# Kernel tuning notes

Hardware: AMD Instinct MI355X
Metric: run time of the kernel (lower is better)

The kernel has to match this reference:

```python
import jax, jax.numpy as jnp
import numpy as np

IN_CH, HID = 602, 256
N0, N1, N2 = 256000, 10240, 1024
E1, E2 = 256000, 10240


def setup_inputs() -> dict:
    key = jax.random.key(0)
    ks = jax.random.split(key, 12)
    x = jax.random.normal(ks[0], (N0, IN_CH), dtype=jnp.float32)
    src1 = jax.random.randint(ks[1], (E1,), 0, N0)
    dst1 = jax.random.randint(ks[2], (E1,), 0, N1)
    src2 = jax.random.randint(ks[3], (E2,), 0, N1)
    dst2 = jax.random.randint(ks[4], (E2,), 0, N2)
    s1 = 1.0 / np.sqrt(IN_CH)
    s2 = 1.0 / np.sqrt(HID)
    W1l = jax.random.normal(ks[5], (IN_CH, HID), dtype=jnp.float32) * s1
    W1r = jax.random.normal(ks[6], (IN_CH, HID), dtype=jnp.float32) * s1
    b1 = jax.random.normal(ks[7], (HID,), dtype=jnp.float32) * s1
    W2l = jax.random.normal(ks[8], (HID, HID), dtype=jnp.float32) * s2
    W2r = jax.random.normal(ks[9], (HID, HID), dtype=jnp.float32) * s2
    b2 = jax.random.normal(ks[10], (HID,), dtype=jnp.float32) * s2
    return {"x": x, "src1": src1, "dst1": dst1, "src2": src2, "dst2": dst2,
            "W1l": W1l, "b1": b1, "W1r": W1r, "W2l": W2l, "b2": b2, "W2r": W2r,
            "n1": N1, "n2": N2}


def _sage_mean(x_src, x_tgt, src, dst, Wl, bl, Wr, n_tgt):
    # gather neighbor (source) features, mean-aggregate to targets
    msg = x_src[src]  # [E, C]
    ssum = jax.ops.segment_sum(msg, dst, num_segments=n_tgt)
    cnt = jax.ops.segment_sum(jnp.ones((src.shape[0], 1), x_src.dtype), dst,
                              num_segments=n_tgt)
    agg = ssum / jnp.maximum(cnt, 1.0)  # isolated targets get 0 (PyG scatter-mean)
    # SAGEConv: lin_l(agg) (with bias) + lin_r(x_root) (no bias)
    return agg @ Wl + bl + x_tgt @ Wr


def reference(x, src1, dst1, src2, dst2, W1l, b1, W1r, W2l, b2, W2r, n1, n2):
    h = _sage_mean(x, x[:n1], src1, dst1, W1l, b1, W1r, n1)
    h = jax.nn.relu(h)  # dropout p=0.5 is identity in eval mode
    out = _sage_mean(h, h[:n2], src2, dst2, W2l, b2, W2r, n2)
    return out
```

## Files before the change

kernel.cpp:

```cpp
#include <hip/hip_runtime.h>
#include <hip/hip_bf16.h>

#define IN_CH 602
#define HID 256
#define N0C 256000
#define N1C 10240
#define N2C 1024
#define E1C 256000
#define E2C 10240
#define K1 1216
#define K2 512

typedef __bf16 bf16x8 __attribute__((ext_vector_type(8)));
typedef float f32x4 __attribute__((ext_vector_type(4)));
typedef unsigned short u16;


__global__ void hist_kernel(const int* __restrict__ dst, int* __restrict__ cnt, int E) {
    int i = blockIdx.x * blockDim.x + threadIdx.x;
    if (i < E) atomicAdd(&cnt[dst[i]], 1);
}

__global__ void scan_kernel(const int* __restrict__ cnt, int* __restrict__ offs,
                            int* __restrict__ cursor, int n) {
    __shared__ int part[256];
    int tid = threadIdx.x;
    int chunk = n >> 8;
    int lo = tid * chunk;
    int s = 0;
    for (int i = 0; i < chunk; i++) s += cnt[lo + i];
    part[tid] = s;
    __syncthreads();
    for (int d = 1; d < 256; d <<= 1) {
        int v = (tid >= d) ? part[tid - d] : 0;
        __syncthreads();
        part[tid] += v;
        __syncthreads();
    }
    int run = part[tid] - s;
    for (int i = 0; i < chunk; i++) {
        offs[lo + i] = run;
        cursor[lo + i] = run;
        run += cnt[lo + i];
    }
}

__global__ void fill_kernel(const int* __restrict__ src, const int* __restrict__ dst,
                            int* __restrict__ cursor, int* __restrict__ eidx, int E) {
    int i = blockIdx.x * blockDim.x + threadIdx.x;
    if (i < E) {
        int p = atomicAdd(&cursor[dst[i]], 1);
        eidx[p] = src[i];
    }
}


__global__ void build_bt_kernel(const float* __restrict__ Wl, const float* __restrict__ Wr,
                                __hip_bfloat16* __restrict__ Bt, int Kin, int Kpad) {
    int idx = blockIdx.x * blockDim.x + threadIdx.x;
    int total = HID * Kpad;
    if (idx >= total) return;
    int n = idx / Kpad, k = idx - n * Kpad;
    float v = 0.f;
    if (k < Kin)            v = Wl[k * HID + n];
    else if (k < 2 * Kin)   v = Wr[(k - Kin) * HID + n];
    Bt[(size_t)n * Kpad + k] = __float2bfloat16(v);
}


__global__ void agg1_kernel(const float* __restrict__ x, const int* __restrict__ cnt,
                            const int* __restrict__ offs, const int* __restrict__ eidx,
                            __hip_bfloat16* __restrict__ A1) {
    int t = blockIdx.x;
    int tid = threadIdx.x;
    int deg = cnt[t];
    int base = offs[t];
    float a0 = 0.f, a1 = 0.f, a2 = 0.f;
    for (int i = 0; i < deg; i++) {
        const float* row = x + (size_t)eidx[base + i] * IN_CH;
        a0 += row[tid];
        if (tid < IN_CH - 256) a1 += row[tid + 256];
        if (tid < IN_CH - 512) a2 += row[tid + 512];
    }
    float inv = 1.0f / (float)(deg > 0 ? deg : 1);
    __hip_bfloat16* d = A1 + (size_t)t * K1;
    d[tid] = __float2bfloat16(a0 * inv);
    if (tid < IN_CH - 256) d[tid + 256] = __float2bfloat16(a1 * inv);
    if (tid < IN_CH - 512) d[tid + 512] = __float2bfloat16(a2 * inv);
    const float* xr = x + (size_t)t * IN_CH;
    d[IN_CH + tid] = __float2bfloat16(xr[tid]);
    if (tid < IN_CH - 256) d[IN_CH + tid + 256] = __float2bfloat16(xr[tid + 256]);
    if (tid < IN_CH - 512) d[IN_CH + tid + 512] = __float2bfloat16(xr[tid + 512]);
    if (tid < K1 - 2 * IN_CH) d[2 * IN_CH + tid] = __float2bfloat16(0.f);
}


__global__ void agg2_kernel(const __hip_bfloat16* __restrict__ h, const int* __restrict__ cnt,
                            const int* __restrict__ offs, const int* __restrict__ eidx,
                            __hip_bfloat16* __restrict__ A2) {
    int t = blockIdx.x, tid = threadIdx.x;
    int deg = cnt[t], base = offs[t];
    float acc = 0.f;
    for (int i = 0; i < deg; i++)
        acc += __bfloat162float(h[(size_t)eidx[base + i] * HID + tid]);
    float inv = 1.0f / (float)(deg > 0 ? deg : 1);
    A2[(size_t)t * K2 + tid] = __float2bfloat16(acc * inv);
    A2[(size_t)t * K2 + HID + tid] = h[(size_t)t * HID + tid];
}


template <int K, bool RELU, bool OUT_BF16>
__global__ __launch_bounds__(256) void gemm_kernel(const __hip_bfloat16* __restrict__ A,
                                                   const __hip_bfloat16* __restrict__ Bt,
                                                   const float* __restrict__ bias,
                                                   void* __restrict__ Cout) {
    __shared__ __align__(16) u16 As[128 * 40];
    __shared__ __align__(16) u16 Bs[128 * 40];
    int tid = threadIdx.x;
    int m0 = blockIdx.x * 128;
    int n0 = blockIdx.y * 128;
    int wave = tid >> 6, lane = tid & 63;
    int wm = (wave & 1) * 64, wn = (wave >> 1) * 64;
    int lm = lane & 15, quad = lane >> 4;
    int k8 = quad * 8;
    int sr = tid >> 2;
    int sc = (tid & 3) * 8;
    const u16* Au = (const u16*)A;
    const u16* Bu = (const u16*)Bt;

    f32x4 acc[4][4];
#pragma unroll
    for (int i = 0; i < 4; i++)
#pragma unroll
        for (int j = 0; j < 4; j++) acc[i][j] = (f32x4){0.f, 0.f, 0.f, 0.f};

    for (int kt = 0; kt < K; kt += 32) {
#pragma unroll
        for (int hh = 0; hh < 2; hh++) {
            int r = sr + 64 * hh;
            *(uint4*)&As[r * 40 + sc] = *(const uint4*)&Au[(size_t)(m0 + r) * K + kt + sc];
            *(uint4*)&Bs[r * 40 + sc] = *(const uint4*)&Bu[(size_t)(n0 + r) * K + kt + sc];
        }
        __syncthreads();
        bf16x8 a[4], b[4];
#pragma unroll
        for (int i = 0; i < 4; i++) a[i] = *(const bf16x8*)&As[(wm + i * 16 + lm) * 40 + k8];
#pragma unroll
        for (int j = 0; j < 4; j++) b[j] = *(const bf16x8*)&Bs[(wn + j * 16 + lm) * 40 + k8];
#pragma unroll
        for (int i = 0; i < 4; i++)
#pragma unroll
            for (int j = 0; j < 4; j++)
                acc[i][j] = __builtin_amdgcn_mfma_f32_16x16x32_bf16(a[i], b[j], acc[i][j], 0, 0, 0);
        __syncthreads();
    }

#pragma unroll
    for (int i = 0; i < 4; i++) {
#pragma unroll
        for (int j = 0; j < 4; j++) {
            int n = n0 + wn + j * 16 + lm;
            float bv = bias[n];
#pragma unroll
            for (int r = 0; r < 4; r++) {
                int m = m0 + wm + i * 16 + quad * 4 + r;
                float v = acc[i][j][r] + bv;
                if (RELU) v = fmaxf(v, 0.f);
                if (OUT_BF16)
                    ((__hip_bfloat16*)Cout)[(size_t)m * HID + n] = __float2bfloat16(v);
                else
                    ((float*)Cout)[(size_t)m * HID + n] = v;
            }
        }
    }
}


extern "C" void kernel_launch(void* const* d_in, const int* in_sizes, int n_in,
                              void* d_out, int out_size, void* d_ws, size_t ws_size,
                              hipStream_t stream) {
    const float* x   = (const float*)d_in[0];
    const int* src1  = (const int*)d_in[1];
    const int* dst1  = (const int*)d_in[2];
    const int* src2  = (const int*)d_in[3];
    const int* dst2  = (const int*)d_in[4];
    const float* W1l = (const float*)d_in[5];
    const float* b1  = (const float*)d_in[6];
    const float* W1r = (const float*)d_in[7];
    const float* W2l = (const float*)d_in[8];
    const float* b2  = (const float*)d_in[9];
    const float* W2r = (const float*)d_in[10];

    char* ws = (char*)d_ws;
    size_t off = 0;
    auto carve = [&](size_t bytes) -> char* {
        char* p = ws + off;
        off += (bytes + 255) & ~(size_t)255;
        return p;
    };
    __hip_bfloat16* A1  = (__hip_bfloat16*)carve((size_t)N1C * K1 * 2);
    __hip_bfloat16* Bt1 = (__hip_bfloat16*)carve((size_t)HID * K1 * 2);
    __hip_bfloat16* h   = (__hip_bfloat16*)carve((size_t)N1C * HID * 2);
    __hip_bfloat16* A2  = (__hip_bfloat16*)carve((size_t)N2C * K2 * 2);
    __hip_bfloat16* Bt2 = (__hip_bfloat16*)carve((size_t)HID * K2 * 2);
    int* cnt1  = (int*)carve(N1C * 4);
    int* offs1 = (int*)carve(N1C * 4);
    int* cur1  = (int*)carve(N1C * 4);
    int* eidx1 = (int*)carve((size_t)E1C * 4);
    int* cnt2  = (int*)carve(N2C * 4);
    int* offs2 = (int*)carve(N2C * 4);
    int* cur2  = (int*)carve(N2C * 4);
    int* eidx2 = (int*)carve((size_t)E2C * 4);

    hipMemsetAsync(cnt1, 0, N1C * 4, stream);
    hipMemsetAsync(cnt2, 0, N2C * 4, stream);
    hist_kernel<<<(E1C + 255) / 256, 256, 0, stream>>>(dst1, cnt1, E1C);
    hist_kernel<<<(E2C + 255) / 256, 256, 0, stream>>>(dst2, cnt2, E2C);
    scan_kernel<<<1, 256, 0, stream>>>(cnt1, offs1, cur1, N1C);
    scan_kernel<<<1, 256, 0, stream>>>(cnt2, offs2, cur2, N2C);
    fill_kernel<<<(E1C + 255) / 256, 256, 0, stream>>>(src1, dst1, cur1, eidx1, E1C);
    fill_kernel<<<(E2C + 255) / 256, 256, 0, stream>>>(src2, dst2, cur2, eidx2, E2C);
    build_bt_kernel<<<(HID * K1 + 255) / 256, 256, 0, stream>>>(W1l, W1r, Bt1, IN_CH, K1);
    build_bt_kernel<<<(HID * K2 + 255) / 256, 256, 0, stream>>>(W2l, W2r, Bt2, HID, K2);
    agg1_kernel<<<N1C, 256, 0, stream>>>(x, cnt1, offs1, eidx1, A1);
    gemm_kernel<K1, true, true><<<dim3(N1C / 128, 2), 256, 0, stream>>>(A1, Bt1, b1, h);
    agg2_kernel<<<N2C, 256, 0, stream>>>(h, cnt2, offs2, eidx2, A2);
    gemm_kernel<K2, false, false><<<dim3(N2C / 128, 2), 256, 0, stream>>>(A2, Bt2, b2, d_out);
}
```

Measured before the change: 969.3 us.

## Merge preprocessing launches, vectorize agg1 gather, register-prefetch GEMM tiles

Merges the paired histogram, scan, fill and weight-transpose launches into single launches and replaces the memsets with one zeroing kernel, cutting launch overhead. agg1 now stages neighbor indices in shared memory, gathers float2 rows with 4-way unrolling and writes packed bf16 pairs, giving more memory-level parallelism in the dominant gather. The GEMM prefetches the next K tile into registers while the current tile is computed, overlapping global loads with MFMA. The prefetch adds register pressure. The float2 loads rely on each row being 8-byte aligned, which holds because 602 is even.

```diff
diff --git a/kernel.cpp b/kernel.cpp
--- a/kernel.cpp
+++ b/kernel.cpp
@@ -14,15 +14,34 @@
 typedef __bf16 bf16x8 __attribute__((ext_vector_type(8)));
 typedef float f32x4 __attribute__((ext_vector_type(4)));
 typedef unsigned short u16;
-
-
-__global__ void hist_kernel(const int* __restrict__ dst, int* __restrict__ cnt, int E) {
+typedef unsigned int u32;
+
+static __device__ __forceinline__ u32 pack_bf16(float a, float b) {
+    __hip_bfloat16 lo = __float2bfloat16(a), hi = __float2bfloat16(b);
+    u16 ul = *(u16*)&lo, uh = *(u16*)&hi;
+    return (u32)ul | ((u32)uh << 16);
+}
+
+
+__global__ void zero_cnt_kernel(int* __restrict__ cnt1, int* __restrict__ cnt2) {
     int i = blockIdx.x * blockDim.x + threadIdx.x;
-    if (i < E) atomicAdd(&cnt[dst[i]], 1);
-}
-
-__global__ void scan_kernel(const int* __restrict__ cnt, int* __restrict__ offs,
-                            int* __restrict__ cursor, int n) {
+    if (i < N1C) cnt1[i] = 0;
+    else if (i < N1C + N2C) cnt2[i - N1C] = 0;
+}
+
+__global__ void hist_kernel(const int* __restrict__ dst1, int* __restrict__ cnt1,
+                            const int* __restrict__ dst2, int* __restrict__ cnt2) {
+    int i = blockIdx.x * blockDim.x + threadIdx.x;
+    if (i < E1C) atomicAdd(&cnt1[dst1[i]], 1);
+    else if (i < E1C + E2C) atomicAdd(&cnt2[dst2[i - E1C]], 1);
+}
+
+__global__ void scan_kernel(const int* __restrict__ cnt1, int* __restrict__ offs1, int* __restrict__ cur1,
+                            const int* __restrict__ cnt2, int* __restrict__ offs2, int* __restrict__ cur2) {
+    const int* cnt = blockIdx.x ? cnt2 : cnt1;
+    int* offs = blockIdx.x ? offs2 : offs1;
+    int* cursor = blockIdx.x ? cur2 : cur1;
+    int n = blockIdx.x ? N2C : N1C;
     __shared__ int part[256];
     int tid = threadIdx.x;
     int chunk = n >> 8;
@@ -45,21 +64,38 @@
     }
 }
 
-__global__ void fill_kernel(const int* __restrict__ src, const int* __restrict__ dst,
-                            int* __restrict__ cursor, int* __restrict__ eidx, int E) {
+__global__ void fill_kernel(const int* __restrict__ src1, const int* __restrict__ dst1,
+                            int* __restrict__ cur1, int* __restrict__ eidx1,
+                            const int* __restrict__ src2, const int* __restrict__ dst2,
+                            int* __restrict__ cur2, int* __restrict__ eidx2) {
     int i = blockIdx.x * blockDim.x + threadIdx.x;
-    if (i < E) {
-        int p = atomicAdd(&cursor[dst[i]], 1);
-        eidx[p] = src[i];
-    }
-}
-
-
-__global__ void build_bt_kernel(const float* __restrict__ Wl, const float* __restrict__ Wr,
-                                __hip_bfloat16* __restrict__ Bt, int Kin, int Kpad) {
+    if (i < E1C) {
+        int p = atomicAdd(&cur1[dst1[i]], 1);
+        eidx1[p] = src1[i];
+    } else if (i < E1C + E2C) {
+        int j = i - E1C;
+        int p = atomicAdd(&cur2[dst2[j]], 1);
+        eidx2[p] = src2[j];
+    }
+}
+
+
+__global__ void build_bt_kernel(const float* __restrict__ W1l, const float* __restrict__ W1r,
+                                __hip_bfloat16* __restrict__ Bt1,
+                                const float* __restrict__ W2l, const float* __restrict__ W2r,
+                                __hip_bfloat16* __restrict__ Bt2) {
     int idx = blockIdx.x * blockDim.x + threadIdx.x;
-    int total = HID * Kpad;
-    if (idx >= total) return;
+    const int total1 = HID * K1;
+    const float *Wl, *Wr;
+    __hip_bfloat16* Bt;
+    int Kin, Kpad;
+    if (idx < total1) {
+        Wl = W1l; Wr = W1r; Bt = Bt1; Kin = IN_CH; Kpad = K1;
+    } else {
+        idx -= total1;
+        if (idx >= HID * K2) return;
+        Wl = W2l; Wr = W2r; Bt = Bt2; Kin = HID; Kpad = K2;
+    }
     int n = idx / Kpad, k = idx - n * Kpad;
     float v = 0.f;
     if (k < Kin)            v = Wl[k * HID + n];
@@ -68,30 +104,65 @@
 }
 
 
-__global__ void agg1_kernel(const float* __restrict__ x, const int* __restrict__ cnt,
-                            const int* __restrict__ offs, const int* __restrict__ eidx,
-                            __hip_bfloat16* __restrict__ A1) {
-    int t = blockIdx.x;
-    int tid = threadIdx.x;
-    int deg = cnt[t];
-    int base = offs[t];
-    float a0 = 0.f, a1 = 0.f, a2 = 0.f;
-    for (int i = 0; i < deg; i++) {
-        const float* row = x + (size_t)eidx[base + i] * IN_CH;
-        a0 += row[tid];
-        if (tid < IN_CH - 256) a1 += row[tid + 256];
-        if (tid < IN_CH - 512) a2 += row[tid + 512];
-    }
+__global__ __launch_bounds__(256) void agg1_kernel(const float* __restrict__ x,
+                                                   const int* __restrict__ cnt,
+                                                   const int* __restrict__ offs,
+                                                   const int* __restrict__ eidx,
+                                                   u16* __restrict__ A1) {
+    __shared__ int nbr[256];
+    int t = blockIdx.x, tid = threadIdx.x;
+    int deg = cnt[t], base = offs[t];
+    const bool has2 = tid < (301 - 256);
+    float2 s0 = {0.f, 0.f}, s1 = {0.f, 0.f};
+
+    for (int c0 = 0; c0 < deg; c0 += 256) {
+        int n = deg - c0;
+        if (n > 256) n = 256;
+        __syncthreads();
+        if (tid < n) nbr[tid] = eidx[base + c0 + tid];
+        __syncthreads();
+        int i = 0;
+        for (; i + 4 <= n; i += 4) {
+            const float2* r0 = (const float2*)(x + (size_t)nbr[i + 0] * IN_CH);
+            const float2* r1 = (const float2*)(x + (size_t)nbr[i + 1] * IN_CH);
+            const float2* r2 = (const float2*)(x + (size_t)nbr[i + 2] * IN_CH);
+            const float2* r3 = (const float2*)(x + (size_t)nbr[i + 3] * IN_CH);
+            float2 v0 = r0[tid], v1 = r1[tid], v2 = r2[tid], v3 = r3[tid];
+            float2 w0, w1, w2, w3;
+            if (has2) {
+                w0 = r0[tid + 256]; w1 = r1[tid + 256];
+                w2 = r2[tid + 256]; w3 = r3[tid + 256];
+            }
+            s0.x += v0.x + v1.x; s0.y += v0.y + v1.y;
+            s0.x += v2.x + v3.x; s0.y += v2.y + v3.y;
+            if (has2) {
+                s1.x += w0.x + w1.x; s1.y += w0.y + w1.y;
+                s1.x += w2.x + w3.x; s1.y += w2.y + w3.y;
+            }
+        }
+        for (; i < n; i++) {
+            const float2* r0 = (const float2*)(x + (size_t)nbr[i] * IN_CH);
+            float2 v0 = r0[tid];
+            s0.x += v0.x; s0.y += v0.y;
+            if (has2) {
+                float2 w0 = r0[tid + 256];
+                s1.x += w0.x; s1.y += w0.y;
+            }
+        }
+    }
+
     float inv = 1.0f / (float)(deg > 0 ? deg : 1);
-    __hip_bfloat16* d = A1 + (size_t)t * K1;
-    d[tid] = __float2bfloat16(a0 * inv);
-    if (tid < IN_CH - 256) d[tid + 256] = __float2bfloat16(a1 * inv);
-    if (tid < IN_CH - 512) d[tid + 512] = __float2bfloat16(a2 * inv);
-    const float* xr = x + (size_t)t * IN_CH;
-    d[IN_CH + tid] = __float2bfloat16(xr[tid]);
-    if (tid < IN_CH - 256) d[IN_CH + tid + 256] = __float2bfloat16(xr[tid + 256]);
-    if (tid < IN_CH - 512) d[IN_CH + tid + 512] = __float2bfloat16(xr[tid + 512]);
-    if (tid < K1 - 2 * IN_CH) d[2 * IN_CH + tid] = __float2bfloat16(0.f);
+    u16* d = A1 + (size_t)t * K1;
+    *(u32*)&d[2 * tid] = pack_bf16(s0.x * inv, s0.y * inv);
+    if (has2) *(u32*)&d[2 * (tid + 256)] = pack_bf16(s1.x * inv, s1.y * inv);
+    const float2* xr = (const float2*)(x + (size_t)t * IN_CH);
+    float2 v = xr[tid];
+    *(u32*)&d[602 + 2 * tid] = pack_bf16(v.x, v.y);
+    if (has2) {
+        float2 w = xr[tid + 256];
+        *(u32*)&d[602 + 2 * (tid + 256)] = pack_bf16(w.x, w.y);
+    }
+    if (tid < 6) *(u32*)&d[1204 + 2 * tid] = 0u;
 }
 
 
@@ -134,14 +205,27 @@
 #pragma unroll
         for (int j = 0; j < 4; j++) acc[i][j] = (f32x4){0.f, 0.f, 0.f, 0.f};
 
+    uint4 ra0, ra1, rb0, rb1;
+    {
+        ra0 = *(const uint4*)&Au[(size_t)(m0 + sr) * K + sc];
+        ra1 = *(const uint4*)&Au[(size_t)(m0 + sr + 64) * K + sc];
+        rb0 = *(const uint4*)&Bu[(size_t)(n0 + sr) * K + sc];
+        rb1 = *(const uint4*)&Bu[(size_t)(n0 + sr + 64) * K + sc];
+    }
+
     for (int kt = 0; kt < K; kt += 32) {
-#pragma unroll
-        for (int hh = 0; hh < 2; hh++) {
-            int r = sr + 64 * hh;
-            *(uint4*)&As[r * 40 + sc] = *(const uint4*)&Au[(size_t)(m0 + r) * K + kt + sc];
-            *(uint4*)&Bs[r * 40 + sc] = *(const uint4*)&Bu[(size_t)(n0 + r) * K + kt + sc];
+        *(uint4*)&As[sr * 40 + sc] = ra0;
+        *(uint4*)&As[(sr + 64) * 40 + sc] = ra1;
+        *(uint4*)&Bs[sr * 40 + sc] = rb0;
+        *(uint4*)&Bs[(sr + 64) * 40 + sc] = rb1;
+        __syncthreads();
+        if (kt + 32 < K) {
+            int kn = kt + 32;
+            ra0 = *(const uint4*)&Au[(size_t)(m0 + sr) * K + kn + sc];
+            ra1 = *(const uint4*)&Au[(size_t)(m0 + sr + 64) * K + kn + sc];
+            rb0 = *(const uint4*)&Bu[(size_t)(n0 + sr) * K + kn + sc];
+            rb1 = *(const uint4*)&Bu[(size_t)(n0 + sr + 64) * K + kn + sc];
         }
-        __syncthreads();
         bf16x8 a[4], b[4];
 #pragma unroll
         for (int i = 0; i < 4; i++) a[i] = *(const bf16x8*)&As[(wm + i * 16 + lm) * 40 + k8];
@@ -212,17 +296,13 @@
     int* cur2  = (int*)carve(N2C * 4);
     int* eidx2 = (int*)carve((size_t)E2C * 4);
 
-    hipMemsetAsync(cnt1, 0, N1C * 4, stream);
-    hipMemsetAsync(cnt2, 0, N2C * 4, stream);
-    hist_kernel<<<(E1C + 255) / 256, 256, 0, stream>>>(dst1, cnt1, E1C);
-    hist_kernel<<<(E2C + 255) / 256, 256, 0, stream>>>(dst2, cnt2, E2C);
-    scan_kernel<<<1, 256, 0, stream>>>(cnt1, offs1, cur1, N1C);
-    scan_kernel<<<1, 256, 0, stream>>>(cnt2, offs2, cur2, N2C);
-    fill_kernel<<<(E1C + 255) / 256, 256, 0, stream>>>(src1, dst1, cur1, eidx1, E1C);
-    fill_kernel<<<(E2C + 255) / 256, 256, 0, stream>>>(src2, dst2, cur2, eidx2, E2C);
-    build_bt_kernel<<<(HID * K1 + 255) / 256, 256, 0, stream>>>(W1l, W1r, Bt1, IN_CH, K1);
-    build_bt_kernel<<<(HID * K2 + 255) / 256, 256, 0, stream>>>(W2l, W2r, Bt2, HID, K2);
-    agg1_kernel<<<N1C, 256, 0, stream>>>(x, cnt1, offs1, eidx1, A1);
+    zero_cnt_kernel<<<(N1C + N2C + 255) / 256, 256, 0, stream>>>(cnt1, cnt2);
+    hist_kernel<<<(E1C + E2C + 255) / 256, 256, 0, stream>>>(dst1, cnt1, dst2, cnt2);
+    scan_kernel<<<2, 256, 0, stream>>>(cnt1, offs1, cur1, cnt2, offs2, cur2);
+    fill_kernel<<<(E1C + E2C + 255) / 256, 256, 0, stream>>>(src1, dst1, cur1, eidx1,
+                                                             src2, dst2, cur2, eidx2);
+    build_bt_kernel<<<(HID * K1 + HID * K2 + 255) / 256, 256, 0, stream>>>(W1l, W1r, Bt1, W2l, W2r, Bt2);
+    agg1_kernel<<<N1C, 256, 0, stream>>>(x, cnt1, offs1, eidx1, (u16*)A1);
     gemm_kernel<K1, true, true><<<dim3(N1C / 128, 2), 256, 0, stream>>>(A1, Bt1, b1, h);
     agg2_kernel<<<N2C, 256, 0, stream>>>(h, cnt2, offs2, eidx2, A2);
     gemm_kernel<K2, false, false><<<dim3(N2C / 128, 2), 256, 0, stream>>>(A2, Bt2, b2, d_out);
```

Measured after the change: 894.6 us. 1.08x faster.
